# Optimization experiments

Hardware: AMD Instinct MI355X
Metric: run time of the kernel (lower is better)

Reference implementation:

```python
import jax, jax.numpy as jnp
import numpy as np

IN_DIM = 768
OUT_DIM = 768


def setup_inputs() -> dict:
    key = jax.random.key(0)
    k_x, k_q, k_k, k_v = jax.random.split(key, 4)
    B, S = 4, 4096
    x = jax.random.normal(k_x, (B, S, IN_DIM), dtype=jnp.float32)
    scale = 1.0 / np.sqrt(IN_DIM)
    Wq = jax.random.normal(k_q, (IN_DIM, OUT_DIM), dtype=jnp.float32) * scale
    Wk = jax.random.normal(k_k, (IN_DIM, OUT_DIM), dtype=jnp.float32) * scale
    Wv = jax.random.normal(k_v, (IN_DIM, OUT_DIM), dtype=jnp.float32) * scale
    return {"x": x, "Wq": Wq, "Wk": Wk, "Wv": Wv}


def reference(x, Wq, Wk, Wv):
    # x: [B, S, D_in]; W*: [D_in, D_out] (Linear without bias)
    q = jnp.einsum('bsd,de->bse', x, Wq)
    k = jnp.einsum('bsd,de->bse', x, Wk)
    v = jnp.einsum('bsd,de->bse', x, Wv)
    S = x.shape[1]
    scores = jnp.einsum('bqe,bke->bqk', q, k)  # [B, S, S]
    causal = jnp.tril(jnp.ones((S, S), dtype=bool))  # True where allowed
    scores = jnp.where(causal[None], scores, -jnp.inf)
    scale = 1.0 / jnp.sqrt(jnp.asarray(q.shape[-1], dtype=scores.dtype))
    weights = jax.nn.softmax(scores * scale, axis=-1)
    # dropout p=0.0 -> identity
    return jnp.einsum('bqk,bke->bqe', weights, v)
```

## Files before the change

### kernel.cpp

```cpp
#include <hip/hip_runtime.h>
#include <hip/hip_bf16.h>
#include <hip/hip_fp16.h>

#define DIM 768
#define SLEN 4096
#define BATCH 4
#define NTILES 528
#define NT256 136
#define SPB ((size_t)NTILES * 16384)

typedef __attribute__((ext_vector_type(8))) short short8;
typedef __attribute__((ext_vector_type(4))) short short4v;
typedef __attribute__((ext_vector_type(4))) float f32x4;
typedef __attribute__((ext_vector_type(8))) _Float16 f16x8;

typedef __attribute__((address_space(1))) void gvoid;
typedef __attribute__((address_space(3))) void lvoid;

__device__ __forceinline__ void gl_lds16(const void* g, void* l) {
  __builtin_amdgcn_global_load_lds((gvoid*)g, (lvoid*)l, 16, 0, 0);
}

__device__ __forceinline__ unsigned short f2h(float x) {
  union { _Float16 h; unsigned short u; } c; c.h = (_Float16)x; return c.u;
}
__device__ __forceinline__ float h2f(unsigned short u) {
  union { _Float16 h; unsigned short u; } c; c.u = u; return (float)c.h;
}

union V8 { short8 v; unsigned short u[8]; };

__global__ __launch_bounds__(256) void convert_x_kernel(
    const float* __restrict__ x, unsigned short* __restrict__ xb) {
  size_t i = ((size_t)blockIdx.x * 256 + threadIdx.x) * 8;
  f32x4 a = *(const f32x4*)(x + i);
  f32x4 b = *(const f32x4*)(x + i + 4);
  V8 o;
#pragma unroll
  for (int j = 0; j < 4; ++j) { o.u[j] = f2h(a[j]); o.u[4 + j] = f2h(b[j]); }
  *(short8*)(xb + i) = o.v;
}

__global__ __launch_bounds__(256) void transpose_w_kernel(
    const float* __restrict__ Wq, const float* __restrict__ Wk,
    const float* __restrict__ Wv, unsigned short* __restrict__ Wt) {
  __shared__ float Tl[32][33];
  const float* Wi = blockIdx.z == 0 ? Wq : (blockIdx.z == 1 ? Wk : Wv);
  unsigned short* Wo = Wt + (size_t)blockIdx.z * DIM * DIM;
  int k0 = blockIdx.x * 32, n0 = blockIdx.y * 32;
  int t = threadIdx.x;
  int r = t >> 3, c4 = (t & 7) * 4;
  f32x4 v = *(const f32x4*)(Wi + (size_t)(k0 + r) * DIM + n0 + c4);
#pragma unroll
  for (int j = 0; j < 4; ++j) Tl[r][c4 + j] = v[j];
  __syncthreads();
  short4v ov;
#pragma unroll
  for (int j = 0; j < 4; ++j) ov[j] = (short)f2h(Tl[c4 + j][r]);
  *(short4v*)(Wo + (size_t)(n0 + r) * DIM + k0 + c4) = ov;
}


#define STAGE(src, row0, kb, ldsoff)                                              \
  {                                                                               \
    gl_lds16((src) + (size_t)((row0) + rA) * DIM + (kb) + cA,                     \
             ldsb + (ldsoff) + t * 16);                                           \
    gl_lds16((src) + (size_t)((row0) + 64 + rA) * DIM + (kb) + cA,                \
             ldsb + (ldsoff) + 8192 + t * 16);                                    \
  }

#define STAGEP(srcp, stride, ldsoff)                                              \
  {                                                                               \
    gl_lds16((srcp) + (size_t)rA * (stride) + cA, ldsb + (ldsoff) + t * 16);      \
    gl_lds16((srcp) + (size_t)(64 + rA) * (stride) + cA,                          \
             ldsb + (ldsoff) + 8192 + t * 16);                                    \
  }

#define RDA(dst, base, chb)                                                       \
  _Pragma("unroll") for (int j = 0; j < 4; ++j)                                   \
      dst[j] = __builtin_bit_cast(f16x8, *(const short8*)(ldsb + (base) +         \
               (j * 32 + arow) * 128 + (chb)));

#define RDB(dst, base, chb)                                                       \
  _Pragma("unroll") for (int n = 0; n < 4; ++n)                                   \
      dst[n] = __builtin_bit_cast(f16x8, *(const short8*)(ldsb + (base) +         \
               bh * 16384 + (brow + n * 16) * 128 + (chb)));

#define MFMA16(af, bf, FO)                                                        \
  __builtin_amdgcn_s_setprio(1);                                                  \
  _Pragma("unroll") for (int j = 0; j < 4; ++j)                                   \
    _Pragma("unroll") for (int n = 0; n < 4; ++n)                                 \
      acc[(FO) + j][n] = __builtin_amdgcn_mfma_f32_16x16x32_f16(                  \
          af[j], bf[n], acc[(FO) + j][n], 0, 0, 0);                               \
  __builtin_amdgcn_s_setprio(0);

#define LGKM(N)                                                                   \
  asm volatile("s_waitcnt lgkmcnt(" #N ")" ::: "memory");                         \
  __builtin_amdgcn_sched_barrier(0);

#define TILE_BODY(aBx, bBx, STGB, STGA)                                           \
  {                                                                               \
    f16x8 a0_[4], a1_[4], a2_[4], a3_[4], b0_[4], b2_[4];                         \
    RDA(a0_, (aBx), ch0);                                                         \
    RDB(b0_, (bBx), ch0);                                                         \
    RDA(a1_, (aBx) + 16384, ch0);                                                 \
    STGB;                                                                         \
    LGKM(4); MFMA16(a0_, b0_, 0);                                                 \
    RDA(a2_, (aBx), ch0 ^ 64);                                                    \
    RDB(b2_, (bBx), ch0 ^ 64);                                                    \
    STGA;                                                                         \
    LGKM(8); MFMA16(a1_, b0_, 4);                                                 \
    RDA(a3_, (aBx) + 16384, ch0 ^ 64);                                            \
    LGKM(4); MFMA16(a2_, b2_, 0);                                                 \
    LGKM(0); MFMA16(a3_, b2_, 4);                                                 \
    asm volatile("s_waitcnt vmcnt(0)" ::: "memory");                              \
    asm volatile("s_barrier" ::: "memory");                                       \
  }

template <int MODE>
__global__ __launch_bounds__(512, 2) void gemm8_kernel(
    const unsigned short* __restrict__ Ag, const unsigned short* __restrict__ Bg,
    unsigned short* __restrict__ o0, unsigned short* __restrict__ o1,
    unsigned short* __restrict__ o2, size_t stAB, size_t stS) {
  __shared__ __align__(16) unsigned short lds[65536];
  char* ldsb = (char*)lds;
  const int t = threadIdx.x;
  const int lane = t & 63, w = t >> 6;
  const int l15 = lane & 15, lg = lane >> 4;
  const int wr = w >> 2, wc = w & 3;

  int m0, n0, qt = 0, kt = 0, z = 0;
  const unsigned short *A, *B;
  unsigned short* Co = nullptr;
  unsigned short* Sb = nullptr;
  if (MODE == 0) {
    const int o = blockIdx.x;
    const int oi = (o & 7) * 72 + (o >> 3);
    const int mt = oi / 9, sub = oi - mt * 9;
    const int ntile = sub / 3;
    z = sub - ntile * 3;
    if (z < 2) {
      m0 = mt * 256; n0 = ntile * 256;
      A = Ag; B = Bg + (size_t)z * DIM * DIM;
      Co = z == 0 ? o0 : o1;
    } else {
      m0 = ntile * 256; n0 = mt * 256;
      A = Bg + (size_t)2 * DIM * DIM; B = Ag;
      Co = o2;
    }
  } else {
    const int i0 = blockIdx.x, b = blockIdx.y;
    const int i = (i0 & 7) * 17 + (i0 >> 3);
    qt = (int)((sqrtf(8.f * i + 1.f) - 1.f) * 0.5f);
    while ((qt + 1) * (qt + 2) / 2 <= i) ++qt;
    while (qt * (qt + 1) / 2 > i) --qt;
    kt = i - qt * (qt + 1) / 2;
    m0 = qt * 256; n0 = kt * 256;
    A = Ag + (size_t)b * stAB; B = Bg + (size_t)b * stAB;
    Sb = o0 + (size_t)b * stS;
  }

  const int rA = t >> 3;
  const int cA = (((t & 7) ^ ((t >> 3) & 7)) << 3);
  const int ch0 = ((lg ^ (l15 & 7)) << 4);
  const int arow = wr * 16 + l15;
  const int bh = wc >> 1;
  const int brow = (wc & 1) * 64 + l15;

  f32x4 acc[8][4];
#pragma unroll
  for (int f = 0; f < 8; ++f)
#pragma unroll
    for (int n = 0; n < 4; ++n) acc[f][n] = f32x4{0.f, 0.f, 0.f, 0.f};

  STAGE(A, m0, 0, 0);
  STAGE(A, m0 + 128, 0, 16384);
  STAGE(B, n0, 0, 65536);
  STAGE(B, n0 + 128, 0, 65536 + 16384);
  asm volatile("s_waitcnt vmcnt(0)" ::: "memory");
  asm volatile("s_barrier" ::: "memory");

  for (int tt = 0; tt < 12; ++tt) {
    const int bt = tt & 1;
    const int aB = bt * 32768;
    const int bB = 65536 + bt * 32768;
    const int aN = (1 - bt) * 32768;
    const int bN = 65536 + (1 - bt) * 32768;
    const int kb1 = (tt + 1 < 12 ? tt + 1 : 11) * 64;
    TILE_BODY(aB, bB,
              STAGE(B, n0, kb1, bN); STAGE(B, n0 + 128, kb1, bN + 16384),
              STAGE(A, m0, kb1, aN); STAGE(A, m0 + 128, kb1, aN + 16384));
  }

  if (MODE == 0) {
    if (z < 2) {
#pragma unroll
      for (int f = 0; f < 8; ++f) {
        const int row = m0 + f * 32 + wr * 16 + lg * 4;
#pragma unroll
        for (int n = 0; n < 4; ++n) {
          const int col = n0 + wc * 64 + n * 16 + l15;
#pragma unroll
          for (int ii = 0; ii < 4; ++ii)
            Co[(size_t)(row + ii) * DIM + col] = f2h(acc[f][n][ii]);
        }
      }
    } else {
      const int bb = n0 >> 12;
      unsigned short* O = Co + (size_t)bb * DIM * SLEN;
#pragma unroll
      for (int f = 0; f < 8; ++f) {
        const int row = m0 + f * 32 + wr * 16 + lg * 4;
#pragma unroll
        for (int n = 0; n < 4; ++n) {
          const int sl = (n0 + wc * 64 + n * 16 + l15) & (SLEN - 1);
#pragma unroll
          for (int ii = 0; ii < 4; ++ii)
            O[(size_t)(row + ii) * SLEN + sl] = f2h(acc[f][n][ii]);
        }
      }
    }
  } else {
#pragma unroll
    for (int f = 0; f < 8; ++f) {
      const int rl = (f * 32 + wr * 16 + lg * 4) & 127;
      const int Q128 = qt * 2 + (f >= 4 ? 1 : 0);
      const int K128 = kt * 2 + (wc >> 1);
      if (K128 > Q128) continue;
      const size_t tb = (size_t)(Q128 * (Q128 + 1) / 2 + K128) * 16384;
#pragma unroll
      for (int n = 0; n < 4; ++n) {
        const int cl = ((wc & 1) * 64 + n * 16 + l15);
#pragma unroll
        for (int ii = 0; ii < 4; ++ii)
          Sb[tb + (size_t)(rl + ii) * 128 + cl] = f2h(acc[f][n][ii]);
      }
    }
  }
}

__global__ __launch_bounds__(256) void softmax_kernel(
    unsigned short* __restrict__ S, size_t s_bstride) {
  __shared__ float redm[4], reds[4];
  const int r = blockIdx.x, b = blockIdx.y;
  unsigned short* Sb = S + (size_t)b * s_bstride;
  const int qt = r >> 7, rl = r & 127;
  const int ncols = (qt + 1) * 128;
  const size_t rowbase = (size_t)(qt * (qt + 1) / 2) * 16384 + (size_t)rl * 128;
  const int t = threadIdx.x, lane = t & 63, w = t >> 6;
  const int c0 = t * 16;
  const bool act = c0 < ncols;
  const float NEG = -3.0e38f;
  float sv[16];
  unsigned short* p = nullptr;
  if (act) {
    int ktile = c0 >> 7, cl = c0 & 127;
    p = Sb + rowbase + (size_t)ktile * 16384 + cl;
    V8 v0, v1; v0.v = *(const short8*)p; v1.v = *(const short8*)(p + 8);
#pragma unroll
    for (int j = 0; j < 8; ++j) {
      sv[j] = (c0 + j > r) ? NEG : h2f(v0.u[j]);
      sv[8 + j] = (c0 + 8 + j > r) ? NEG : h2f(v1.u[j]);
    }
  } else {
#pragma unroll
    for (int j = 0; j < 16; ++j) sv[j] = NEG;
  }
  float mx = NEG;
#pragma unroll
  for (int j = 0; j < 16; ++j) mx = fmaxf(mx, sv[j]);
#pragma unroll
  for (int d = 1; d < 64; d <<= 1) mx = fmaxf(mx, __shfl_xor(mx, d));
  if (lane == 0) redm[w] = mx;
  __syncthreads();
  mx = fmaxf(fmaxf(redm[0], redm[1]), fmaxf(redm[2], redm[3]));
  const float scl = 1.4426950408889634f / 27.712812921102035f;
  float e[16], sm = 0.f;
#pragma unroll
  for (int j = 0; j < 16; ++j) { e[j] = exp2f((sv[j] - mx) * scl); sm += e[j]; }
#pragma unroll
  for (int d = 1; d < 64; d <<= 1) sm += __shfl_xor(sm, d);
  if (lane == 0) reds[w] = sm;
  __syncthreads();
  float inv = 1.0f / (reds[0] + reds[1] + reds[2] + reds[3]);
  if (act) {
    V8 o0, o1;
#pragma unroll
    for (int j = 0; j < 8; ++j) { o0.u[j] = f2h(e[j] * inv); o1.u[j] = f2h(e[8 + j] * inv); }
    *(short8*)p = o0.v;
    *(short8*)(p + 8) = o1.v;
  }
}

__global__ __launch_bounds__(256) void zero_tile_kernel(unsigned short* __restrict__ z) {
  ((short8*)z)[blockIdx.x * 256 + threadIdx.x] = short8{0, 0, 0, 0, 0, 0, 0, 0};
}

__device__ const int pv_mt[24]  = {15,15,7,14,14,13,13,6,12,12,11,11,5,10,10,9,9,4,8,8,3,2,1,0};
__device__ const int pv_ks0[24] = {0,32,0,0,30,0,28,0,0,26,0,24,0,0,22,0,20,0,0,18,0,0,0,0};
__device__ const int pv_kl[24]  = {32,32,32,30,30,28,28,28,26,26,24,24,24,22,22,20,20,20,18,18,16,12,8,4};
__device__ const int pv_sec[24] = {0,1,0,0,1,0,1,0,0,1,0,1,0,0,1,0,1,0,0,1,0,0,0,0};

__global__ __launch_bounds__(512, 2) void pv256_kernel(
    const unsigned short* __restrict__ S, const unsigned short* __restrict__ Vt,
    const unsigned short* __restrict__ Zt, float* __restrict__ Out,
    float* __restrict__ Part) {
  __shared__ __align__(16) unsigned short lds[65536];
  char* ldsb = (char*)lds;
  const int t = threadIdx.x, lane = t & 63, w = t >> 6;
  const int l15 = lane & 15, lg = lane >> 4;
  const int wr = w >> 2, wc = w & 3;
  const int rank = blockIdx.x / 12, sub = blockIdx.x % 12;
  const int b = sub / 3, nt = sub % 3;
  const int mt = pv_mt[rank], ks0 = pv_ks0[rank], kl = pv_kl[rank];
  const int sec = pv_sec[rank];
  const int q0 = 2 * mt, q1 = 2 * mt + 1;
  const int kend = ks0 + kl;
  const unsigned short* Sbb = S + (size_t)b * SPB;
  const unsigned short* Vb = Vt + (size_t)b * DIM * SLEN + (size_t)(nt * 256) * SLEN;

  auto asrc = [&](int ks, int qh) -> const unsigned short* {
    const int K128 = ks >> 1;
    const unsigned short* base =
        (K128 <= qh) ? Sbb + (size_t)(qh * (qh + 1) / 2 + K128) * 16384 : Zt;
    return base + (ks & 1) * 64;
  };

  const int rA = t >> 3;
  const int cA = (((t & 7) ^ ((t >> 3) & 7)) << 3);
  const int ch0 = ((lg ^ (l15 & 7)) << 4);
  const int arow = wr * 16 + l15;
  const int bh = wc >> 1;
  const int brow = (wc & 1) * 64 + l15;

  f32x4 acc[8][4];
#pragma unroll
  for (int f = 0; f < 8; ++f)
#pragma unroll
    for (int n = 0; n < 4; ++n) acc[f][n] = f32x4{0.f, 0.f, 0.f, 0.f};

  STAGEP(asrc(ks0, q0), 128, 0);
  STAGEP(asrc(ks0, q1), 128, 16384);
  STAGEP(Vb + (size_t)ks0 * 64, SLEN, 65536);
  STAGEP(Vb + (size_t)128 * SLEN + (size_t)ks0 * 64, SLEN, 65536 + 16384);
  asm volatile("s_waitcnt vmcnt(0)" ::: "memory");
  asm volatile("s_barrier" ::: "memory");

  for (int it = 0; it < kl; ++it) {
    const int ts = ks0 + it;
    const int bt = it & 1;
    const int aB = bt * 32768;
    const int bB = 65536 + bt * 32768;
    const int aN = (1 - bt) * 32768;
    const int bN = 65536 + (1 - bt) * 32768;
    const int t1 = (ts + 1 < kend) ? ts + 1 : kend - 1;
    TILE_BODY(aB, bB,
              STAGEP(Vb + (size_t)t1 * 64, SLEN, bN);
              STAGEP(Vb + (size_t)128 * SLEN + (size_t)t1 * 64, SLEN, bN + 16384),
              STAGEP(asrc(t1, q0), 128, aN);
              STAGEP(asrc(t1, q1), 128, aN + 16384));
  }

  if (!sec) {
    float* Ob = Out + (size_t)b * SLEN * DIM + (size_t)(mt * 256) * DIM + nt * 256;
#pragma unroll
    for (int f = 0; f < 8; ++f) {
      const int rl = f * 32 + wr * 16 + lg * 4;
#pragma unroll
      for (int n = 0; n < 4; ++n) {
        const int cl = wc * 64 + n * 16 + l15;
#pragma unroll
        for (int ii = 0; ii < 4; ++ii)
          Ob[(size_t)(rl + ii) * DIM + cl] = acc[f][n][ii];
      }
    }
  } else {
    float* Pb = Part + (size_t)((b * 3 + nt) * 8 + (mt - 8)) * 65536;
#pragma unroll
    for (int f = 0; f < 8; ++f) {
      const int rl = f * 32 + wr * 16 + lg * 4;
#pragma unroll
      for (int n = 0; n < 4; ++n) {
        const int cl = wc * 64 + n * 16 + l15;
#pragma unroll
        for (int ii = 0; ii < 4; ++ii)
          Pb[(size_t)(rl + ii) * 256 + cl] = acc[f][n][ii];
      }
    }
  }
}

__global__ __launch_bounds__(256) void pv_reduce_kernel(
    const float* __restrict__ Part, float* __restrict__ Out) {
  const int bx = blockIdx.x;
  const int p = bx >> 6;
  const int within = ((bx & 63) * 256 + threadIdx.x) * 4;
  const int mt = 8 + (p & 7);
  const int bnt = p >> 3, b = bnt / 3, nt = bnt % 3;
  const int r = within >> 8, c = within & 255;
  float* o = Out + (size_t)b * SLEN * DIM + (size_t)(mt * 256 + r) * DIM + nt * 256 + c;
  const f32x4 pv = *(const f32x4*)(Part + (size_t)p * 65536 + within);
  const f32x4 ov = *(const f32x4*)o;
  *(f32x4*)o = ov + pv;
}

__global__ __launch_bounds__(256) void gemm_pv_kernel(
    const unsigned short* __restrict__ S, const unsigned short* __restrict__ Vt,
    float* __restrict__ Out, size_t s_bstride, int nb) {
  __shared__ __align__(16) unsigned short As[4096], Bs[4096];
  const int idx = blockIdx.x;
  const int qtr = idx / (6 * nb);
  const int rem = idx - qtr * 6 * nb;
  const int b = rem / 6, nt = rem % 6;
  const int qt = 31 - qtr;
  const unsigned short* Sb = S + (size_t)b * s_bstride + (size_t)(qt * (qt + 1) / 2) * 16384;
  const unsigned short* Vb = Vt + (size_t)b * DIM * SLEN + (size_t)(nt * 128) * SLEN;
  float* Ob = Out + (size_t)b * SLEN * DIM + (size_t)(qt * 128) * DIM + nt * 128;
  const int t = threadIdx.x, lane = t & 63, w = t >> 6;
  const int l15 = lane & 15, lg = lane >> 4;
  const int wm = w >> 1, wn = w & 1;
  f32x4 acc[4][4];
#pragma unroll
  for (int a = 0; a < 4; ++a)
#pragma unroll
    for (int b2 = 0; b2 < 4; ++b2) acc[a][b2] = f32x4{0.f, 0.f, 0.f, 0.f};
  const int c0 = t, c1 = t + 256;
  const int r0 = c0 >> 2, k80 = (c0 & 3) * 8;
  const int r1 = c1 >> 2, k81 = (c1 & 3) * 8;
  const int ksteps = (qt + 1) * 4;
  for (int ks = 0; ks < ksteps; ++ks) {
    const int kb = ks * 32;
    const size_t atile = (size_t)(kb >> 7) * 16384 + (size_t)(kb & 127);
    __syncthreads();
    gl_lds16(Sb + atile + (size_t)r0 * 128 + k80, As + (size_t)c0 * 8);
    gl_lds16(Sb + atile + (size_t)r1 * 128 + k81, As + (size_t)c1 * 8);
    gl_lds16(Vb + (size_t)r0 * SLEN + kb + k80, Bs + (size_t)c0 * 8);
    gl_lds16(Vb + (size_t)r1 * SLEN + kb + k81, Bs + (size_t)c1 * 8);
    __syncthreads();
    f16x8 a[4], bf[4];
#pragma unroll
    for (int mi = 0; mi < 4; ++mi)
      a[mi] = __builtin_bit_cast(f16x8, *(const short8*)(As + (wm * 64 + mi * 16 + l15) * 32 + lg * 8));
#pragma unroll
    for (int ni = 0; ni < 4; ++ni)
      bf[ni] = __builtin_bit_cast(f16x8, *(const short8*)(Bs + (wn * 64 + ni * 16 + l15) * 32 + lg * 8));
#pragma unroll
    for (int mi = 0; mi < 4; ++mi)
#pragma unroll
      for (int ni = 0; ni < 4; ++ni)
        acc[mi][ni] = __builtin_amdgcn_mfma_f32_16x16x32_f16(a[mi], bf[ni], acc[mi][ni], 0, 0, 0);
  }
#pragma unroll
  for (int mi = 0; mi < 4; ++mi)
#pragma unroll
    for (int ni = 0; ni < 4; ++ni)
#pragma unroll
      for (int ii = 0; ii < 4; ++ii) {
        int rl = wm * 64 + mi * 16 + lg * 4 + ii;
        int cl = wn * 64 + ni * 16 + l15;
        Ob[(size_t)rl * DIM + cl] = acc[mi][ni][ii];
      }
}

extern "C" void kernel_launch(void* const* d_in, const int* in_sizes, int n_in,
                              void* d_out, int out_size, void* d_ws, size_t ws_size,
                              hipStream_t stream) {
  const float* x  = (const float*)d_in[0];
  const float* Wq = (const float*)d_in[1];
  const float* Wk = (const float*)d_in[2];
  const float* Wv = (const float*)d_in[3];
  float* out = (float*)d_out;

  const size_t n_x = (size_t)BATCH * SLEN * DIM;
  unsigned short* Q  = (unsigned short*)d_ws;
  unsigned short* K  = Q + n_x;
  unsigned short* Vt = K + n_x;
  unsigned short* xb = Vt + n_x;
  unsigned short* wt = xb + n_x;
  const size_t base_elems = 4 * n_x + (size_t)3 * DIM * DIM;
  const bool full = ws_size >= (base_elems + 4 * SPB) * 2;

  convert_x_kernel<<<dim3((unsigned)(n_x / 8 / 256)), 256, 0, stream>>>(x, xb);
  transpose_w_kernel<<<dim3(DIM / 32, DIM / 32, 3), 256, 0, stream>>>(Wq, Wk, Wv, wt);

  gemm8_kernel<0><<<dim3(576), 512, 0, stream>>>(xb, wt, Q, K, Vt, 0, 0);

  if (full) {
    unsigned short* S = (unsigned short*)d_ws + base_elems;
    zero_tile_kernel<<<8, 256, 0, stream>>>(wt);
    gemm8_kernel<1><<<dim3(NT256, BATCH), 512, 0, stream>>>(
        Q, K, S, nullptr, nullptr, (size_t)SLEN * DIM, SPB);
    softmax_kernel<<<dim3(SLEN, BATCH), 256, 0, stream>>>(S, SPB);
    pv256_kernel<<<dim3(288), 512, 0, stream>>>(S, Vt, wt, out, (float*)xb);
    pv_reduce_kernel<<<dim3(6144), 256, 0, stream>>>((const float*)xb, out);
  } else {
    unsigned short* S = xb;
    for (int b = 0; b < BATCH; ++b) {
      const size_t qo = (size_t)b * SLEN * DIM;
      gemm8_kernel<1><<<dim3(NT256, 1), 512, 0, stream>>>(
          Q + qo, K + qo, S, nullptr, nullptr, 0, 0);
      softmax_kernel<<<dim3(SLEN, 1), 256, 0, stream>>>(S, 0);
      gemm_pv_kernel<<<dim3(32 * 6), 256, 0, stream>>>(
          S, Vt + (size_t)b * DIM * SLEN, out + qo, 0, 1);
    }
  }
}
```

Measured before the change: 278.3 us.

## Switch GEMM and PV kernels to K=32 tiles with triple-buffered LDS pipeline

Replaces the double-buffered K=64 staging with a three-stage ring of K=32 tiles, so two tiles are in flight and the wait before each barrier is a partial vmcnt(4) rather than a full drain. LDS use drops from 128KB to 96KB per block. The LDS swizzle and warp-to-tile mapping also change: each warp row now owns a contiguous 128-row half, which makes the causal store a per-warp check instead of a per-fragment one. In exchange there are twice as many iterations and barriers, each doing half the MFMA work, which could expose more synchronisation overhead.

```diff
diff --git a/kernel.cpp b/kernel.cpp
--- a/kernel.cpp
+++ b/kernel.cpp
@@ -61,68 +61,70 @@
 }
 
 
-#define STAGE(src, row0, kb, ldsoff)                                              \
-  {                                                                               \
-    gl_lds16((src) + (size_t)((row0) + rA) * DIM + (kb) + cA,                     \
-             ldsb + (ldsoff) + t * 16);                                           \
-    gl_lds16((src) + (size_t)((row0) + 64 + rA) * DIM + (kb) + cA,                \
-             ldsb + (ldsoff) + 8192 + t * 16);                                    \
-  }
-
-#define STAGEP(srcp, stride, ldsoff)                                              \
-  {                                                                               \
-    gl_lds16((srcp) + (size_t)rA * (stride) + cA, ldsb + (ldsoff) + t * 16);      \
-    gl_lds16((srcp) + (size_t)(64 + rA) * (stride) + cA,                          \
-             ldsb + (ldsoff) + 8192 + t * 16);                                    \
-  }
-
-#define RDA(dst, base, chb)                                                       \
+#define STAGEH(srcp, stride, ldsoff)                                              \
+  gl_lds16((srcp) + (size_t)(t >> 2) * (stride) + cH, ldsb + (ldsoff) + t * 16);
+
+#define STG_AB(Aptr, Bptr, stride, OFF)                                           \
+  STAGEH((Aptr), (stride), (OFF));                                                \
+  STAGEH((Aptr) + 128 * (stride), (stride), (OFF) + 8192);                        \
+  STAGEH((Bptr), (stride), (OFF) + 16384);                                        \
+  STAGEH((Bptr) + 128 * (stride), (stride), (OFF) + 24576);
+
+#define STG_PV(pa0, pa1, Bptr, OFF)                                               \
+  STAGEH((pa0), 128, (OFF));                                                      \
+  STAGEH((pa1), 128, (OFF) + 8192);                                               \
+  STAGEH((Bptr), SLEN, (OFF) + 16384);                                            \
+  STAGEH((Bptr) + 128 * SLEN, SLEN, (OFF) + 24576);
+
+#define RD_A(dst, aoff)                                                           \
   _Pragma("unroll") for (int j = 0; j < 4; ++j)                                   \
-      dst[j] = __builtin_bit_cast(f16x8, *(const short8*)(ldsb + (base) +         \
-               (j * 32 + arow) * 128 + (chb)));
-
-#define RDB(dst, base, chb)                                                       \
+      dst[j] = __builtin_bit_cast(f16x8,                                          \
+               *(const short8*)(ldsb + arb + (aoff) + j * 1024));
+
+#define RD_B(dst, boff)                                                           \
   _Pragma("unroll") for (int n = 0; n < 4; ++n)                                   \
-      dst[n] = __builtin_bit_cast(f16x8, *(const short8*)(ldsb + (base) +         \
-               bh * 16384 + (brow + n * 16) * 128 + (chb)));
-
-#define MFMA16(af, bf, FO)                                                        \
-  __builtin_amdgcn_s_setprio(1);                                                  \
-  _Pragma("unroll") for (int j = 0; j < 4; ++j)                                   \
-    _Pragma("unroll") for (int n = 0; n < 4; ++n)                                 \
-      acc[(FO) + j][n] = __builtin_amdgcn_mfma_f32_16x16x32_f16(                  \
-          af[j], bf[n], acc[(FO) + j][n], 0, 0, 0);                               \
-  __builtin_amdgcn_s_setprio(0);
+      dst[n] = __builtin_bit_cast(f16x8,                                          \
+               *(const short8*)(ldsb + brb + (boff) + n * 1024));
 
 #define LGKM(N)                                                                   \
   asm volatile("s_waitcnt lgkmcnt(" #N ")" ::: "memory");                         \
   __builtin_amdgcn_sched_barrier(0);
 
-#define TILE_BODY(aBx, bBx, STGB, STGA)                                           \
+#define TILE32(AOFF, STG, VMW, BAR)                                               \
   {                                                                               \
-    f16x8 a0_[4], a1_[4], a2_[4], a3_[4], b0_[4], b2_[4];                         \
-    RDA(a0_, (aBx), ch0);                                                         \
-    RDB(b0_, (bBx), ch0);                                                         \
-    RDA(a1_, (aBx) + 16384, ch0);                                                 \
-    STGB;                                                                         \
-    LGKM(4); MFMA16(a0_, b0_, 0);                                                 \
-    RDA(a2_, (aBx), ch0 ^ 64);                                                    \
-    RDB(b2_, (bBx), ch0 ^ 64);                                                    \
-    STGA;                                                                         \
-    LGKM(8); MFMA16(a1_, b0_, 4);                                                 \
-    RDA(a3_, (aBx) + 16384, ch0 ^ 64);                                            \
-    LGKM(4); MFMA16(a2_, b2_, 0);                                                 \
-    LGKM(0); MFMA16(a3_, b2_, 4);                                                 \
-    asm volatile("s_waitcnt vmcnt(0)" ::: "memory");                              \
-    asm volatile("s_barrier" ::: "memory");                                       \
-  }
+    f16x8 fb_[4], fl_[4], fh_[4];                                                 \
+    RD_B(fb_, (AOFF) + 16384);                                                    \
+    RD_A(fl_, (AOFF));                                                            \
+    STG;                                                                          \
+    RD_A(fh_, (AOFF) + 4096);                                                     \
+    LGKM(4);                                                                      \
+    __builtin_amdgcn_s_setprio(1);                                                \
+    _Pragma("unroll") for (int j = 0; j < 4; ++j)                                 \
+      _Pragma("unroll") for (int n = 0; n < 4; ++n)                               \
+        acc[j][n] = __builtin_amdgcn_mfma_f32_16x16x32_f16(                       \
+            fl_[j], fb_[n], acc[j][n], 0, 0, 0);                                  \
+    __builtin_amdgcn_s_setprio(0);                                                \
+    LGKM(0);                                                                      \
+    __builtin_amdgcn_s_setprio(1);                                                \
+    _Pragma("unroll") for (int j = 0; j < 4; ++j)                                 \
+      _Pragma("unroll") for (int n = 0; n < 4; ++n)                               \
+        acc[4 + j][n] = __builtin_amdgcn_mfma_f32_16x16x32_f16(                   \
+            fh_[j], fb_[n], acc[4 + j][n], 0, 0, 0);                              \
+    __builtin_amdgcn_s_setprio(0);                                                \
+    VMW;                                                                          \
+    BAR;                                                                          \
+  }
+
+#define VMC4 asm volatile("s_waitcnt vmcnt(4)" ::: "memory")
+#define VMC0 asm volatile("s_waitcnt vmcnt(0)" ::: "memory")
+#define SBAR asm volatile("s_barrier" ::: "memory")
 
 template <int MODE>
 __global__ __launch_bounds__(512, 2) void gemm8_kernel(
     const unsigned short* __restrict__ Ag, const unsigned short* __restrict__ Bg,
     unsigned short* __restrict__ o0, unsigned short* __restrict__ o1,
     unsigned short* __restrict__ o2, size_t stAB, size_t stS) {
-  __shared__ __align__(16) unsigned short lds[65536];
+  __shared__ __align__(16) unsigned short lds[49152];
   char* ldsb = (char*)lds;
   const int t = threadIdx.x;
   const int lane = t & 63, w = t >> 6;
@@ -160,12 +162,10 @@
     Sb = o0 + (size_t)b * stS;
   }
 
-  const int rA = t >> 3;
-  const int cA = (((t & 7) ^ ((t >> 3) & 7)) << 3);
-  const int ch0 = ((lg ^ (l15 & 7)) << 4);
-  const int arow = wr * 16 + l15;
-  const int bh = wc >> 1;
-  const int brow = (wc & 1) * 64 + l15;
+  const int cH = (((t & 3) ^ ((t >> 3) & 3)) << 3);
+  const int sw = ((lg ^ ((l15 >> 1) & 3)) << 4);
+  const int arb = (wr * 128 + l15) * 64 + sw;
+  const int brb = (wc * 64 + l15) * 64 + sw;
 
   f32x4 acc[8][4];
 #pragma unroll
@@ -173,30 +173,26 @@
 #pragma unroll
     for (int n = 0; n < 4; ++n) acc[f][n] = f32x4{0.f, 0.f, 0.f, 0.f};
 
-  STAGE(A, m0, 0, 0);
-  STAGE(A, m0 + 128, 0, 16384);
-  STAGE(B, n0, 0, 65536);
-  STAGE(B, n0 + 128, 0, 65536 + 16384);
-  asm volatile("s_waitcnt vmcnt(0)" ::: "memory");
-  asm volatile("s_barrier" ::: "memory");
-
-  for (int tt = 0; tt < 12; ++tt) {
-    const int bt = tt & 1;
-    const int aB = bt * 32768;
-    const int bB = 65536 + bt * 32768;
-    const int aN = (1 - bt) * 32768;
-    const int bN = 65536 + (1 - bt) * 32768;
-    const int kb1 = (tt + 1 < 12 ? tt + 1 : 11) * 64;
-    TILE_BODY(aB, bB,
-              STAGE(B, n0, kb1, bN); STAGE(B, n0 + 128, kb1, bN + 16384),
-              STAGE(A, m0, kb1, aN); STAGE(A, m0 + 128, kb1, aN + 16384));
-  }
+  STG_AB(A + (size_t)m0 * DIM + 0, B + (size_t)n0 * DIM + 0, DIM, 0);
+  STG_AB(A + (size_t)m0 * DIM + 32, B + (size_t)n0 * DIM + 32, DIM, 32768);
+  VMC4; SBAR;
+
+  for (int tt = 0; tt < 22; ++tt) {
+    const int bs = (tt % 3) * 32768;
+    const int ts = ((tt + 2) % 3) * 32768;
+    const int kb2 = (tt + 2) * 32;
+    TILE32(bs,
+           STG_AB(A + (size_t)m0 * DIM + kb2, B + (size_t)n0 * DIM + kb2, DIM, ts),
+           VMC4, SBAR);
+  }
+  TILE32((22 % 3) * 32768, (void)0, VMC0, SBAR);
+  TILE32((23 % 3) * 32768, (void)0, (void)0, (void)0);
 
   if (MODE == 0) {
     if (z < 2) {
 #pragma unroll
       for (int f = 0; f < 8; ++f) {
-        const int row = m0 + f * 32 + wr * 16 + lg * 4;
+        const int row = m0 + wr * 128 + f * 16 + lg * 4;
 #pragma unroll
         for (int n = 0; n < 4; ++n) {
           const int col = n0 + wc * 64 + n * 16 + l15;
@@ -210,7 +206,7 @@
       unsigned short* O = Co + (size_t)bb * DIM * SLEN;
 #pragma unroll
       for (int f = 0; f < 8; ++f) {
-        const int row = m0 + f * 32 + wr * 16 + lg * 4;
+        const int row = m0 + wr * 128 + f * 16 + lg * 4;
 #pragma unroll
         for (int n = 0; n < 4; ++n) {
           const int sl = (n0 + wc * 64 + n * 16 + l15) & (SLEN - 1);
@@ -221,19 +217,20 @@
       }
     }
   } else {
-#pragma unroll
-    for (int f = 0; f < 8; ++f) {
-      const int rl = (f * 32 + wr * 16 + lg * 4) & 127;
-      const int Q128 = qt * 2 + (f >= 4 ? 1 : 0);
-      const int K128 = kt * 2 + (wc >> 1);
-      if (K128 > Q128) continue;
+    const int Q128 = qt * 2 + wr;
+    const int K128 = kt * 2 + (wc >> 1);
+    if (K128 <= Q128) {
       const size_t tb = (size_t)(Q128 * (Q128 + 1) / 2 + K128) * 16384;
 #pragma unroll
-      for (int n = 0; n < 4; ++n) {
-        const int cl = ((wc & 1) * 64 + n * 16 + l15);
-#pragma unroll
-        for (int ii = 0; ii < 4; ++ii)
-          Sb[tb + (size_t)(rl + ii) * 128 + cl] = f2h(acc[f][n][ii]);
+      for (int f = 0; f < 8; ++f) {
+        const int rl = f * 16 + lg * 4;
+#pragma unroll
+        for (int n = 0; n < 4; ++n) {
+          const int cl = ((wc & 1) * 64 + n * 16 + l15);
+#pragma unroll
+          for (int ii = 0; ii < 4; ++ii)
+            Sb[tb + (size_t)(rl + ii) * 128 + cl] = f2h(acc[f][n][ii]);
+        }
       }
     }
   }
@@ -297,15 +294,15 @@
 }
 
 __device__ const int pv_mt[24]  = {15,15,7,14,14,13,13,6,12,12,11,11,5,10,10,9,9,4,8,8,3,2,1,0};
-__device__ const int pv_ks0[24] = {0,32,0,0,30,0,28,0,0,26,0,24,0,0,22,0,20,0,0,18,0,0,0,0};
-__device__ const int pv_kl[24]  = {32,32,32,30,30,28,28,28,26,26,24,24,24,22,22,20,20,20,18,18,16,12,8,4};
+__device__ const int pv_ks0[24] = {0,64,0,0,60,0,56,0,0,52,0,48,0,0,44,0,40,0,0,36,0,0,0,0};
+__device__ const int pv_kl[24]  = {64,64,64,60,60,56,56,56,52,52,48,48,48,44,44,40,40,40,36,36,32,24,16,8};
 __device__ const int pv_sec[24] = {0,1,0,0,1,0,1,0,0,1,0,1,0,0,1,0,1,0,0,1,0,0,0,0};
 
 __global__ __launch_bounds__(512, 2) void pv256_kernel(
     const unsigned short* __restrict__ S, const unsigned short* __restrict__ Vt,
     const unsigned short* __restrict__ Zt, float* __restrict__ Out,
     float* __restrict__ Part) {
-  __shared__ __align__(16) unsigned short lds[65536];
+  __shared__ __align__(16) unsigned short lds[49152];
   char* ldsb = (char*)lds;
   const int t = threadIdx.x, lane = t & 63, w = t >> 6;
   const int l15 = lane & 15, lg = lane >> 4;
@@ -315,23 +312,20 @@
   const int mt = pv_mt[rank], ks0 = pv_ks0[rank], kl = pv_kl[rank];
   const int sec = pv_sec[rank];
   const int q0 = 2 * mt, q1 = 2 * mt + 1;
-  const int kend = ks0 + kl;
   const unsigned short* Sbb = S + (size_t)b * SPB;
   const unsigned short* Vb = Vt + (size_t)b * DIM * SLEN + (size_t)(nt * 256) * SLEN;
 
   auto asrc = [&](int ks, int qh) -> const unsigned short* {
-    const int K128 = ks >> 1;
+    const int K128 = ks >> 2;
     const unsigned short* base =
         (K128 <= qh) ? Sbb + (size_t)(qh * (qh + 1) / 2 + K128) * 16384 : Zt;
-    return base + (ks & 1) * 64;
+    return base + (ks & 3) * 32;
   };
 
-  const int rA = t >> 3;
-  const int cA = (((t & 7) ^ ((t >> 3) & 7)) << 3);
-  const int ch0 = ((lg ^ (l15 & 7)) << 4);
-  const int arow = wr * 16 + l15;
-  const int bh = wc >> 1;
-  const int brow = (wc & 1) * 64 + l15;
+  const int cH = (((t & 3) ^ ((t >> 3) & 3)) << 3);
+  const int sw = ((lg ^ ((l15 >> 1) & 3)) << 4);
+  const int arb = (wr * 128 + l15) * 64 + sw;
+  const int brb = (wc * 64 + l15) * 64 + sw;
 
   f32x4 acc[8][4];
 #pragma unroll
@@ -339,33 +333,26 @@
 #pragma unroll
     for (int n = 0; n < 4; ++n) acc[f][n] = f32x4{0.f, 0.f, 0.f, 0.f};
 
-  STAGEP(asrc(ks0, q0), 128, 0);
-  STAGEP(asrc(ks0, q1), 128, 16384);
-  STAGEP(Vb + (size_t)ks0 * 64, SLEN, 65536);
-  STAGEP(Vb + (size_t)128 * SLEN + (size_t)ks0 * 64, SLEN, 65536 + 16384);
-  asm volatile("s_waitcnt vmcnt(0)" ::: "memory");
-  asm volatile("s_barrier" ::: "memory");
-
-  for (int it = 0; it < kl; ++it) {
-    const int ts = ks0 + it;
-    const int bt = it & 1;
-    const int aB = bt * 32768;
-    const int bB = 65536 + bt * 32768;
-    const int aN = (1 - bt) * 32768;
-    const int bN = 65536 + (1 - bt) * 32768;
-    const int t1 = (ts + 1 < kend) ? ts + 1 : kend - 1;
-    TILE_BODY(aB, bB,
-              STAGEP(Vb + (size_t)t1 * 64, SLEN, bN);
-              STAGEP(Vb + (size_t)128 * SLEN + (size_t)t1 * 64, SLEN, bN + 16384),
-              STAGEP(asrc(t1, q0), 128, aN);
-              STAGEP(asrc(t1, q1), 128, aN + 16384));
-  }
+  STG_PV(asrc(ks0, q0), asrc(ks0, q1), Vb + (size_t)ks0 * 32, 0);
+  STG_PV(asrc(ks0 + 1, q0), asrc(ks0 + 1, q1), Vb + (size_t)(ks0 + 1) * 32, 32768);
+  VMC4; SBAR;
+
+  for (int it = 0; it < kl - 2; ++it) {
+    const int bs = (it % 3) * 32768;
+    const int ts = ((it + 2) % 3) * 32768;
+    const int k2 = ks0 + it + 2;
+    TILE32(bs,
+           STG_PV(asrc(k2, q0), asrc(k2, q1), Vb + (size_t)k2 * 32, ts),
+           VMC4, SBAR);
+  }
+  TILE32(((kl - 2) % 3) * 32768, (void)0, VMC0, SBAR);
+  TILE32(((kl - 1) % 3) * 32768, (void)0, (void)0, (void)0);
 
   if (!sec) {
     float* Ob = Out + (size_t)b * SLEN * DIM + (size_t)(mt * 256) * DIM + nt * 256;
 #pragma unroll
     for (int f = 0; f < 8; ++f) {
-      const int rl = f * 32 + wr * 16 + lg * 4;
+      const int rl = wr * 128 + f * 16 + lg * 4;
 #pragma unroll
       for (int n = 0; n < 4; ++n) {
         const int cl = wc * 64 + n * 16 + l15;
@@ -378,7 +365,7 @@
     float* Pb = Part + (size_t)((b * 3 + nt) * 8 + (mt - 8)) * 65536;
 #pragma unroll
     for (int f = 0; f < 8; ++f) {
-      const int rl = f * 32 + wr * 16 + lg * 4;
+      const int rl = wr * 128 + f * 16 + lg * 4;
 #pragma unroll
       for (int n = 0; n < 4; ++n) {
         const int cl = wc * 64 + n * 16 + l15;
```

Result: slower. 293.1 us (+5.3%).

## Switch GEMM tiles from 16x16x32 to 32x32x16 MFMA with new fragment layout

Applied to the files above, without the earlier changes.

Replaces the 16x16x32 f16 MFMA inner loops with 32x32x16 MFMAs in both the projection/score GEMM and the PV GEMM. Each wave now owns a contiguous 128x64 sub-tile as 4x2 32x32 accumulators, which changes the LDS read addressing, swizzle indexing, wait counts and all epilogue store index math. The larger MFMA is meant to cut LDS fragment reads per flop and raise matrix-core efficiency. In exchange the epilogue stores are scattered differently and the row/column mapping must match the swizzled LDS layout exactly, otherwise results are wrong.

```diff
diff --git a/kernel.cpp b/kernel.cpp
--- a/kernel.cpp
+++ b/kernel.cpp
@@ -12,6 +12,7 @@
 typedef __attribute__((ext_vector_type(8))) short short8;
 typedef __attribute__((ext_vector_type(4))) short short4v;
 typedef __attribute__((ext_vector_type(4))) float f32x4;
+typedef __attribute__((ext_vector_type(16))) float f32x16;
 typedef __attribute__((ext_vector_type(8))) _Float16 f16x8;
 
 typedef __attribute__((address_space(1))) void gvoid;
@@ -76,22 +77,20 @@
              ldsb + (ldsoff) + 8192 + t * 16);                                    \
   }
 
-#define RDA(dst, base, chb)                                                       \
-  _Pragma("unroll") for (int j = 0; j < 4; ++j)                                   \
-      dst[j] = __builtin_bit_cast(f16x8, *(const short8*)(ldsb + (base) +         \
-               (j * 32 + arow) * 128 + (chb)));
-
-#define RDB(dst, base, chb)                                                       \
-  _Pragma("unroll") for (int n = 0; n < 4; ++n)                                   \
-      dst[n] = __builtin_bit_cast(f16x8, *(const short8*)(ldsb + (base) +         \
-               bh * 16384 + (brow + n * 16) * 128 + (chb)));
-
-#define MFMA16(af, bf, FO)                                                        \
+#define RDS(dA, dB, aBx, bBx, C2)                                                 \
+  _Pragma("unroll") for (int f = 0; f < 4; ++f)                                   \
+      dA[f] = __builtin_bit_cast(f16x8, *(const short8*)(ldsb + (aBx) + aFB +     \
+              f * 4096 + (((C2) ^ sb0) << 4)));                                   \
+  _Pragma("unroll") for (int cf = 0; cf < 2; ++cf)                                \
+      dB[cf] = __builtin_bit_cast(f16x8, *(const short8*)(ldsb + (bBx) + bFB +    \
+               cf * 4096 + (((C2) ^ sb0) << 4)));
+
+#define MFMA8(dA, dB)                                                             \
   __builtin_amdgcn_s_setprio(1);                                                  \
-  _Pragma("unroll") for (int j = 0; j < 4; ++j)                                   \
-    _Pragma("unroll") for (int n = 0; n < 4; ++n)                                 \
-      acc[(FO) + j][n] = __builtin_amdgcn_mfma_f32_16x16x32_f16(                  \
-          af[j], bf[n], acc[(FO) + j][n], 0, 0, 0);                               \
+  _Pragma("unroll") for (int f = 0; f < 4; ++f)                                   \
+    _Pragma("unroll") for (int cf = 0; cf < 2; ++cf)                              \
+      acc[f][cf] = __builtin_amdgcn_mfma_f32_32x32x16_f16(                        \
+          dA[f], dB[cf], acc[f][cf], 0, 0, 0);                                    \
   __builtin_amdgcn_s_setprio(0);
 
 #define LGKM(N)                                                                   \
@@ -100,19 +99,18 @@
 
 #define TILE_BODY(aBx, bBx, STGB, STGA)                                           \
   {                                                                               \
-    f16x8 a0_[4], a1_[4], a2_[4], a3_[4], b0_[4], b2_[4];                         \
-    RDA(a0_, (aBx), ch0);                                                         \
-    RDB(b0_, (bBx), ch0);                                                         \
-    RDA(a1_, (aBx) + 16384, ch0);                                                 \
+    f16x8 A0[4], A1[4], A2[4], A3[4];                                             \
+    f16x8 B0[2], B1[2], B2[2], B3[2];                                             \
+    RDS(A0, B0, (aBx), (bBx), 0);                                                 \
+    RDS(A1, B1, (aBx), (bBx), 2);                                                 \
     STGB;                                                                         \
-    LGKM(4); MFMA16(a0_, b0_, 0);                                                 \
-    RDA(a2_, (aBx), ch0 ^ 64);                                                    \
-    RDB(b2_, (bBx), ch0 ^ 64);                                                    \
+    LGKM(6); MFMA8(A0, B0);                                                       \
+    RDS(A2, B2, (aBx), (bBx), 4);                                                 \
     STGA;                                                                         \
-    LGKM(8); MFMA16(a1_, b0_, 4);                                                 \
-    RDA(a3_, (aBx) + 16384, ch0 ^ 64);                                            \
-    LGKM(4); MFMA16(a2_, b2_, 0);                                                 \
-    LGKM(0); MFMA16(a3_, b2_, 4);                                                 \
+    LGKM(6); MFMA8(A1, B1);                                                       \
+    RDS(A3, B3, (aBx), (bBx), 6);                                                 \
+    LGKM(6); MFMA8(A2, B2);                                                       \
+    LGKM(0); MFMA8(A3, B3);                                                       \
     asm volatile("s_waitcnt vmcnt(0)" ::: "memory");                              \
     asm volatile("s_barrier" ::: "memory");                                       \
   }
@@ -126,7 +124,7 @@
   char* ldsb = (char*)lds;
   const int t = threadIdx.x;
   const int lane = t & 63, w = t >> 6;
-  const int l15 = lane & 15, lg = lane >> 4;
+  const int l31 = lane & 31, hb = lane >> 5;
   const int wr = w >> 2, wc = w & 3;
 
   int m0, n0, qt = 0, kt = 0, z = 0;
@@ -162,16 +160,18 @@
 
   const int rA = t >> 3;
   const int cA = (((t & 7) ^ ((t >> 3) & 7)) << 3);
-  const int ch0 = ((lg ^ (l15 & 7)) << 4);
-  const int arow = wr * 16 + l15;
+  const int sb0 = hb ^ (lane & 7);
+  const int aFB = wr * 16384 + l31 * 128;
   const int bh = wc >> 1;
-  const int brow = (wc & 1) * 64 + l15;
-
-  f32x4 acc[8][4];
-#pragma unroll
-  for (int f = 0; f < 8; ++f)
-#pragma unroll
-    for (int n = 0; n < 4; ++n) acc[f][n] = f32x4{0.f, 0.f, 0.f, 0.f};
+  const int bFB = bh * 16384 + (wc & 1) * 8192 + l31 * 128;
+
+  f32x16 acc[4][2];
+#pragma unroll
+  for (int f = 0; f < 4; ++f)
+#pragma unroll
+    for (int cf = 0; cf < 2; ++cf)
+#pragma unroll
+      for (int r = 0; r < 16; ++r) acc[f][cf][r] = 0.f;
 
   STAGE(A, m0, 0, 0);
   STAGE(A, m0 + 128, 0, 16384);
@@ -195,46 +195,47 @@
   if (MODE == 0) {
     if (z < 2) {
 #pragma unroll
-      for (int f = 0; f < 8; ++f) {
-        const int row = m0 + f * 32 + wr * 16 + lg * 4;
-#pragma unroll
-        for (int n = 0; n < 4; ++n) {
-          const int col = n0 + wc * 64 + n * 16 + l15;
-#pragma unroll
-          for (int ii = 0; ii < 4; ++ii)
-            Co[(size_t)(row + ii) * DIM + col] = f2h(acc[f][n][ii]);
+      for (int f = 0; f < 4; ++f)
+#pragma unroll
+        for (int cf = 0; cf < 2; ++cf) {
+          const int col = n0 + wc * 64 + cf * 32 + l31;
+#pragma unroll
+          for (int r = 0; r < 16; ++r) {
+            const int row = m0 + wr * 128 + f * 32 + (r & 3) + 8 * (r >> 2) + 4 * hb;
+            Co[(size_t)row * DIM + col] = f2h(acc[f][cf][r]);
+          }
         }
-      }
     } else {
       const int bb = n0 >> 12;
       unsigned short* O = Co + (size_t)bb * DIM * SLEN;
 #pragma unroll
-      for (int f = 0; f < 8; ++f) {
-        const int row = m0 + f * 32 + wr * 16 + lg * 4;
-#pragma unroll
-        for (int n = 0; n < 4; ++n) {
-          const int sl = (n0 + wc * 64 + n * 16 + l15) & (SLEN - 1);
-#pragma unroll
-          for (int ii = 0; ii < 4; ++ii)
-            O[(size_t)(row + ii) * SLEN + sl] = f2h(acc[f][n][ii]);
+      for (int f = 0; f < 4; ++f)
+#pragma unroll
+        for (int cf = 0; cf < 2; ++cf) {
+          const int sl = (n0 + wc * 64 + cf * 32 + l31) & (SLEN - 1);
+#pragma unroll
+          for (int r = 0; r < 16; ++r) {
+            const int row = m0 + wr * 128 + f * 32 + (r & 3) + 8 * (r >> 2) + 4 * hb;
+            O[(size_t)row * SLEN + sl] = f2h(acc[f][cf][r]);
+          }
         }
-      }
     }
   } else {
-#pragma unroll
-    for (int f = 0; f < 8; ++f) {
-      const int rl = (f * 32 + wr * 16 + lg * 4) & 127;
-      const int Q128 = qt * 2 + (f >= 4 ? 1 : 0);
-      const int K128 = kt * 2 + (wc >> 1);
-      if (K128 > Q128) continue;
+    const int Q128 = qt * 2 + wr;
+    const int K128 = kt * 2 + (wc >> 1);
+    if (K128 <= Q128) {
       const size_t tb = (size_t)(Q128 * (Q128 + 1) / 2 + K128) * 16384;
 #pragma unroll
-      for (int n = 0; n < 4; ++n) {
-        const int cl = ((wc & 1) * 64 + n * 16 + l15);
-#pragma unroll
-        for (int ii = 0; ii < 4; ++ii)
-          Sb[tb + (size_t)(rl + ii) * 128 + cl] = f2h(acc[f][n][ii]);
-      }
+      for (int f = 0; f < 4; ++f)
+#pragma unroll
+        for (int cf = 0; cf < 2; ++cf) {
+          const int cl = (wc & 1) * 64 + cf * 32 + l31;
+#pragma unroll
+          for (int r = 0; r < 16; ++r) {
+            const int rl = f * 32 + (r & 3) + 8 * (r >> 2) + 4 * hb;
+            Sb[tb + (size_t)rl * 128 + cl] = f2h(acc[f][cf][r]);
+          }
+        }
     }
   }
 }
@@ -308,7 +309,7 @@
   __shared__ __align__(16) unsigned short lds[65536];
   char* ldsb = (char*)lds;
   const int t = threadIdx.x, lane = t & 63, w = t >> 6;
-  const int l15 = lane & 15, lg = lane >> 4;
+  const int l31 = lane & 31, hb = lane >> 5;
   const int wr = w >> 2, wc = w & 3;
   const int rank = blockIdx.x / 12, sub = blockIdx.x % 12;
   const int b = sub / 3, nt = sub % 3;
@@ -328,16 +329,18 @@
 
   const int rA = t >> 3;
   const int cA = (((t & 7) ^ ((t >> 3) & 7)) << 3);
-  const int ch0 = ((lg ^ (l15 & 7)) << 4);
-  const int arow = wr * 16 + l15;
+  const int sb0 = hb ^ (lane & 7);
+  const int aFB = wr * 16384 + l31 * 128;
   const int bh = wc >> 1;
-  const int brow = (wc & 1) * 64 + l15;
-
-  f32x4 acc[8][4];
-#pragma unroll
-  for (int f = 0; f < 8; ++f)
-#pragma unroll
-    for (int n = 0; n < 4; ++n) acc[f][n] = f32x4{0.f, 0.f, 0.f, 0.f};
+  const int bFB = bh * 16384 + (wc & 1) * 8192 + l31 * 128;
+
+  f32x16 acc[4][2];
+#pragma unroll
+  for (int f = 0; f < 4; ++f)
+#pragma unroll
+    for (int cf = 0; cf < 2; ++cf)
+#pragma unroll
+      for (int r = 0; r < 16; ++r) acc[f][cf][r] = 0.f;
 
   STAGEP(asrc(ks0, q0), 128, 0);
   STAGEP(asrc(ks0, q1), 128, 16384);
@@ -364,29 +367,29 @@
   if (!sec) {
     float* Ob = Out + (size_t)b * SLEN * DIM + (size_t)(mt * 256) * DIM + nt * 256;
 #pragma unroll
-    for (int f = 0; f < 8; ++f) {
-      const int rl = f * 32 + wr * 16 + lg * 4;
-#pragma unroll
-      for (int n = 0; n < 4; ++n) {
-        const int cl = wc * 64 + n * 16 + l15;
-#pragma unroll
-        for (int ii = 0; ii < 4; ++ii)
-          Ob[(size_t)(rl + ii) * DIM + cl] = acc[f][n][ii];
+    for (int f = 0; f < 4; ++f)
+#pragma unroll
+      for (int cf = 0; cf < 2; ++cf) {
+        const int cl = wc * 64 + cf * 32 + l31;
+#pragma unroll
+        for (int r = 0; r < 16; ++r) {
+          const int rl = wr * 128 + f * 32 + (r & 3) + 8 * (r >> 2) + 4 * hb;
+          Ob[(size_t)rl * DIM + cl] = acc[f][cf][r];
+        }
       }
-    }
   } else {
     float* Pb = Part + (size_t)((b * 3 + nt) * 8 + (mt - 8)) * 65536;
 #pragma unroll
-    for (int f = 0; f < 8; ++f) {
-      const int rl = f * 32 + wr * 16 + lg * 4;
-#pragma unroll
-      for (int n = 0; n < 4; ++n) {
-        const int cl = wc * 64 + n * 16 + l15;
-#pragma unroll
-        for (int ii = 0; ii < 4; ++ii)
-          Pb[(size_t)(rl + ii) * 256 + cl] = acc[f][n][ii];
+    for (int f = 0; f < 4; ++f)
+#pragma unroll
+      for (int cf = 0; cf < 2; ++cf) {
+        const int cl = wc * 64 + cf * 32 + l31;
+#pragma unroll
+        for (int r = 0; r < 16; ++r) {
+          const int rl = wr * 128 + f * 32 + (r & 3) + 8 * (r >> 2) + 4 * hb;
+          Pb[(size_t)rl * 256 + cl] = acc[f][cf][r];
+        }
       }
-    }
   }
 }
 
```

Result: slower. 309.1 us (+11.0%).
